# Performance work log

Hardware: AMD Instinct MI355X
Metric: run time of the kernel (lower is better)

Reference implementation:

```python
import jax, jax.numpy as jnp
import numpy as np
from functools import partial

# ---------------- model dims ----------------
B = 1
CIN = 26
COUT = 26
ED = 128              # embed_dim
MLP_HID = 256         # embed_dim * mlp_ratio (2.0)
NLAT, NLON = 361, 720 # model grid
SF = 4                # scale_factor
H, W = NLAT // SF, NLON // SF   # internal SHT grid (90, 180)
LMAX = H              # 90 spherical-harmonic degrees
MMAX = W // 2 + 1     # 91 azimuthal orders
NB = 4                # num_layers
EPS = 1e-6

# ---------------- spherical harmonic transform setup ----------------
def _legendre(lmax, mmax, theta):
    """Orthonormal associated Legendre P_l^m(cos theta), shape [lmax, mmax, nlat].
    Normalized so that int P^2 sin(theta) dtheta = 1/(2*pi)."""
    ct, st = np.cos(theta), np.sin(theta)
    p = np.zeros((lmax, mmax, theta.shape[0]))
    p[0, 0] = np.sqrt(1.0 / (4.0 * np.pi))
    for m in range(1, min(lmax, mmax)):
        p[m, m] = np.sqrt((2 * m + 1) / (2.0 * m)) * st * p[m - 1, m - 1]
    for m in range(mmax):
        if m + 1 < lmax:
            p[m + 1, m] = np.sqrt(2 * m + 3.0) * ct * p[m, m]
        for l in range(m + 2, lmax):
            a = np.sqrt((4.0 * l * l - 1.0) / (l * l - m * m))
            b = np.sqrt(((l - 1.0) ** 2 - m * m) / (4.0 * (l - 1.0) ** 2 - 1.0))
            p[l, m] = a * (ct * p[l - 1, m] - b * p[l - 2, m])
    return p

def _grid(nlat):
    theta = np.pi * (np.arange(nlat) + 0.5) / nlat   # equiangular midpoints
    w = (np.pi / nlat) * np.sin(theta)               # quadrature weights
    return theta, w

_thf, _wf = _grid(NLAT)
_ths, _ws = _grid(H)
_pf = _legendre(LMAX, MMAX, _thf)
_ps = _legendre(LMAX, MMAX, _ths)
PCT_FULL = jnp.asarray(_pf, jnp.float32)
PCTW_FULL = jnp.asarray(_pf * _wf, jnp.float32)
PCT_SMALL = jnp.asarray(_ps, jnp.float32)
PCTW_SMALL = jnp.asarray(_ps * _ws, jnp.float32)

def _sht(x, pctw, nlon):
    # x: [B,C,nlat,nlon] real -> coeffs [B,C,LMAX,MMAX] complex
    F = jnp.fft.rfft(x, axis=-1)[..., :MMAX] * (2.0 * np.pi / nlon)
    return jnp.einsum('lmt,bctm->bclm', pctw, F)

def _isht(c, pct, nlon):
    # c: [B,C,LMAX,MMAX] complex -> [B,C,nlat_out,nlon] real
    g = jnp.einsum('lmt,bclm->bctm', pct, c)
    return jnp.fft.irfft(g, n=nlon, axis=-1, norm='forward')

# ---------------- elementwise / channel-mixing helpers ----------------
_gelu = partial(jax.nn.gelu, approximate=False)

def _inorm(x, g, b):
    # InstanceNorm2d, affine, eps=1e-6, biased variance over spatial dims
    mu = jnp.mean(x, axis=(-2, -1), keepdims=True)
    var = jnp.var(x, axis=(-2, -1), keepdims=True)
    return (x - mu) * jax.lax.rsqrt(var + EPS) * g[:, None, None] + b[:, None, None]

def _conv1x1(x, w, b=None):
    y = jnp.einsum('oc,bchw->bohw', w, x)
    return y if b is None else y + b[:, None, None]

# ---------------- SFNO forward ----------------
def _forward(x, w_enc0, b_enc0, w_enc1, w_spec_r, w_spec_i, g0, b0, g1, b1,
             w_mlp1, b_mlp1, w_mlp2, b_mlp2, w_skip, w_dec0, b_dec0, w_dec1):
    big_res = x
    # encoder: conv1x1 -> gelu -> conv1x1 (no bias)
    x = _conv1x1(_gelu(_conv1x1(x, w_enc0, b_enc0)), w_enc1)
    # per-block transform configs: first block full->small, last small->full
    fwd_t = [(PCTW_FULL, NLON), (PCTW_SMALL, W), (PCTW_SMALL, W), (PCTW_SMALL, W)]
    inv_t = [(PCT_SMALL, W), (PCT_SMALL, W), (PCT_SMALL, W), (PCT_FULL, NLON)]
    scale_res = [True, False, False, True]
    for i in range(NB):
        pw, nli = fwd_t[i]
        pi, nlo = inv_t[i]
        c = _sht(x, pw, nli)                              # [B,ED,LMAX,MMAX]
        # diagonal-in-l spectral conv (dhconv): complex weight shared over m
        wspec = w_spec_r[i] + 1j * w_spec_i[i]            # [ED,ED,LMAX]
        xf = _isht(jnp.einsum('bilm,oil->bolm', c, wspec), pi, nlo)
        # residual: resample through SHT when grids differ, else identity
        res = _isht(c, pi, nlo) if scale_res[i] else x
        h = _inorm(xf, g0[i], b0[i])                      # norm0 (no inner skip)
        h = _gelu(h)                                      # act_layer0
        h = _conv1x1(_gelu(_conv1x1(h, w_mlp1[i], b_mlp1[i])), w_mlp2[i], b_mlp2[i])
        h = _inorm(h, g1[i], b1[i])                       # norm1
        x = h + _conv1x1(res, w_skip[i])                  # outer_skip='linear'
    # big skip: concat input channels, then decoder
    x = jnp.concatenate([x, big_res], axis=1)
    x = _conv1x1(_gelu(_conv1x1(x, w_dec0, b_dec0)), w_dec1)
    return x

# ---------------- harness ----------------
def setup_inputs() -> dict:
    key = jax.random.key(0)
    ks = jax.random.split(key, 12)
    rn = lambda k, shp, std: jax.random.normal(k, shp, jnp.float32) * std
    return {
        'x': rn(ks[0], (B, CIN, NLAT, NLON), 1.0),
        'w_enc0': rn(ks[1], (ED, CIN), (1.0 / CIN) ** 0.5),
        'b_enc0': jnp.zeros((ED,), jnp.float32),
        'w_enc1': rn(ks[2], (ED, ED), (1.0 / ED) ** 0.5),
        'w_spec_r': rn(ks[3], (NB, ED, ED, LMAX), (1.0 / ED) ** 0.5),
        'w_spec_i': rn(ks[4], (NB, ED, ED, LMAX), (1.0 / ED) ** 0.5),
        'g0': jnp.ones((NB, ED), jnp.float32),
        'b0': jnp.zeros((NB, ED), jnp.float32),
        'g1': jnp.ones((NB, ED), jnp.float32),
        'b1': jnp.zeros((NB, ED), jnp.float32),
        'w_mlp1': rn(ks[5], (NB, MLP_HID, ED), (1.0 / ED) ** 0.5),
        'b_mlp1': jnp.zeros((NB, MLP_HID), jnp.float32),
        'w_mlp2': rn(ks[6], (NB, ED, MLP_HID), (1.0 / MLP_HID) ** 0.5),
        'b_mlp2': jnp.zeros((NB, ED), jnp.float32),
        'w_skip': rn(ks[7], (NB, ED, ED), (0.5 / ED) ** 0.5),
        'w_dec0': rn(ks[8], (ED, ED + CIN), (1.0 / (ED + CIN)) ** 0.5),
        'b_dec0': jnp.zeros((ED,), jnp.float32),
        'w_dec1': rn(ks[9], (COUT, ED), (1.0 / ED) ** 0.5),
    }

def reference(x, w_enc0, b_enc0, w_enc1, w_spec_r, w_spec_i, g0, b0, g1, b1,
              w_mlp1, b_mlp1, w_mlp2, b_mlp2, w_skip, w_dec0, b_dec0, w_dec1):
    return _forward(x, w_enc0, b_enc0, w_enc1, w_spec_r, w_spec_i, g0, b0, g1, b1,
                    w_mlp1, b_mlp1, w_mlp2, b_mlp2, w_skip, w_dec0, b_dec0, w_dec1)
```

## Files before the change

### kernel.cpp

```cpp
#include <hip/hip_runtime.h>
#include <math.h>

#ifndef M_PI
#define M_PI 3.14159265358979323846
#endif

#define NLATF 361
#define NLONF 720
#define HSM 90
#define WSM 180
#define LMX 90
#define MM 91
#define EDIM 128
#define CINN 26
#define MLPH 256
#define PFULL (NLATF*NLONF)
#define PSMALL (HSM*WSM)

__device__ __forceinline__ float geluf(float x){
  return 0.5f*x*(1.0f + erff(x*0.70710678118654752440f));
}

__global__ void legendre_kernel(float* __restrict__ pct, int T){
  int idx = blockIdx.x*blockDim.x + threadIdx.x;
  if (idx >= MM*T) return;
  int m = idx / T, t = idx % T;
  double theta = M_PI*((double)t + 0.5)/T;
  double ct = cos(theta), st = sin(theta);
  double pmm = sqrt(1.0/(4.0*M_PI));
  for (int k=1;k<=m;++k) pmm *= sqrt((2.0*k+1.0)/(2.0*k))*st;
  double prev2 = 0.0, prev = 0.0;
  for (int l=0;l<LMX;++l){
    double v;
    if (l < m) v = 0.0;
    else if (l == m) v = pmm;
    else if (l == m+1) v = sqrt(2.0*m+3.0)*ct*pmm;
    else {
      double ll = l, mm2 = (double)m*m;
      double a = sqrt((4.0*ll*ll-1.0)/(ll*ll-mm2));
      double lm1 = (double)(l-1);
      double b = sqrt((lm1*lm1-mm2)/(4.0*lm1*lm1-1.0));
      v = a*(ct*prev - b*prev2);
    }
    pct[((size_t)l*T + t)*MM + m] = (float)v;
    prev2 = prev; prev = v;
  }
}

__global__ void dft_tables_kernel(float* __restrict__ fcos, float* __restrict__ fsin,
                                  float* __restrict__ icos, float* __restrict__ isin, int N){
  int idx = blockIdx.x*blockDim.x + threadIdx.x;
  if (idx >= N*MM) return;
  int n = idx / MM, m = idx % MM;
  int r = (int)(((long long)n*m) % N);
  double ang = 2.0*M_PI*r/N;
  double c = cos(ang), s = sin(ang);
  fcos[(size_t)n*MM+m] = (float)c;
  fsin[(size_t)n*MM+m] = (float)s;
  double w = (m==0) ? 1.0 : ((2*m==N) ? 1.0 : 2.0);
  icos[(size_t)m*N+n] = (float)(w*c);
  isin[(size_t)m*N+n] = (float)(w*s);
}

__global__ __launch_bounds__(128) void dft_fwd_kernel(
    const float* __restrict__ x, float2* __restrict__ Fw,
    const float* __restrict__ fcos, const float* __restrict__ fsin,
    int T, int N){
  __shared__ float xs[4][NLONF];
  int r0 = blockIdx.x*4;
  const float* xp = x + (size_t)r0*N;
  for (int e=threadIdx.x; e<4*N; e+=128) xs[e/N][e%N] = xp[e];
  __syncthreads();
  int m = threadIdx.x;
  if (m >= MM) return;
  float ar[4] = {0,0,0,0}, ai[4] = {0,0,0,0};
  for (int n=0;n<N;++n){
    float c = fcos[(size_t)n*MM+m], s = fsin[(size_t)n*MM+m];
    #pragma unroll
    for (int r=0;r<4;++r){
      float xv = xs[r][n];
      ar[r] = fmaf(xv, c, ar[r]);
      ai[r] = fmaf(-xv, s, ai[r]);
    }
  }
  #pragma unroll
  for (int r=0;r<4;++r){
    int t = (r0+r) % T;
    float sc = (float)((2.0*M_PI/N)*(M_PI/T)*sin(M_PI*((double)t+0.5)/T));
    Fw[(size_t)(r0+r)*MM+m] = make_float2(ar[r]*sc, ai[r]*sc);
  }
}

__global__ __launch_bounds__(128) void dft_fwd_chunk_kernel(
    const float* __restrict__ x, float2* __restrict__ Fw,
    const float* __restrict__ fcos, const float* __restrict__ fsin,
    int Tc, int t0, int Tfull, int N){
  __shared__ float xs[4][NLONF];
  int r0 = blockIdx.x*4;
  const float* xp = x + (size_t)r0*N;
  for (int e=threadIdx.x; e<4*N; e+=128) xs[e/N][e%N] = xp[e];
  __syncthreads();
  int m = threadIdx.x;
  if (m >= MM) return;
  float ar[4] = {0,0,0,0}, ai[4] = {0,0,0,0};
  for (int n=0;n<N;++n){
    float c = fcos[(size_t)n*MM+m], s = fsin[(size_t)n*MM+m];
    #pragma unroll
    for (int r=0;r<4;++r){
      float xv = xs[r][n];
      ar[r] = fmaf(xv, c, ar[r]);
      ai[r] = fmaf(-xv, s, ai[r]);
    }
  }
  #pragma unroll
  for (int r=0;r<4;++r){
    int rr = r0+r;
    int t = t0 + (rr % Tc);
    float sc = (float)((2.0*M_PI/N)*(M_PI/Tfull)*sin(M_PI*((double)t+0.5)/Tfull));
    Fw[(size_t)rr*MM+m] = make_float2(ar[r]*sc, ai[r]*sc);
  }
}

__global__ __launch_bounds__(192) void leg_fwd_kernel(
    const float2* __restrict__ Fw, float2* __restrict__ cc,
    const float* __restrict__ pct, int T){
  int half = threadIdx.x/96, m = threadIdx.x%96;
  int c0 = blockIdx.x*4;
  int l0 = blockIdx.y*6 + half*3;
  if (m >= MM) return;
  float2 acc[3][4];
  #pragma unroll
  for (int j=0;j<3;++j) for (int c=0;c<4;++c) acc[j][c] = make_float2(0.f,0.f);
  for (int t=0;t<T;++t){
    float p[3];
    #pragma unroll
    for (int j=0;j<3;++j) p[j] = pct[((size_t)(l0+j)*T + t)*MM + m];
    #pragma unroll
    for (int c=0;c<4;++c){
      float2 f = Fw[((size_t)(c0+c)*T + t)*MM + m];
      #pragma unroll
      for (int j=0;j<3;++j){
        acc[j][c].x = fmaf(p[j], f.x, acc[j][c].x);
        acc[j][c].y = fmaf(p[j], f.y, acc[j][c].y);
      }
    }
  }
  #pragma unroll
  for (int j=0;j<3;++j)
    #pragma unroll
    for (int c=0;c<4;++c)
      cc[((size_t)(c0+c)*LMX + (l0+j))*MM + m] = acc[j][c];
}

__global__ __launch_bounds__(192) void leg_fwd_acc_kernel(
    const float2* __restrict__ Fw, float2* __restrict__ cc,
    const float* __restrict__ pct, int Tfull, int t0, int Tc){
  int half = threadIdx.x/96, m = threadIdx.x%96;
  int c0 = blockIdx.x*4;
  int l0 = blockIdx.y*6 + half*3;
  if (m >= MM) return;
  float2 acc[3][4];
  #pragma unroll
  for (int j=0;j<3;++j) for (int c=0;c<4;++c) acc[j][c] = make_float2(0.f,0.f);
  for (int tl=0; tl<Tc; ++tl){
    float p[3];
    #pragma unroll
    for (int j=0;j<3;++j) p[j] = pct[((size_t)(l0+j)*Tfull + t0+tl)*MM + m];
    #pragma unroll
    for (int c=0;c<4;++c){
      float2 f = Fw[((size_t)(c0+c)*Tc + tl)*MM + m];
      #pragma unroll
      for (int j=0;j<3;++j){
        acc[j][c].x = fmaf(p[j], f.x, acc[j][c].x);
        acc[j][c].y = fmaf(p[j], f.y, acc[j][c].y);
      }
    }
  }
  #pragma unroll
  for (int j=0;j<3;++j)
    #pragma unroll
    for (int c=0;c<4;++c){
      size_t idx = ((size_t)(c0+c)*LMX + (l0+j))*MM + m;
      cc[idx].x += acc[j][c].x;
      cc[idx].y += acc[j][c].y;
    }
}

__global__ __launch_bounds__(192) void leg_inv_kernel(
    const float2* __restrict__ cc, float2* __restrict__ g,
    const float* __restrict__ pct, int T){
  int half = threadIdx.x/96, m = threadIdx.x%96;
  int c0 = blockIdx.x*4;
  int t0 = blockIdx.y*6 + half*3;
  if (m >= MM) return;
  float2 acc[3][4];
  #pragma unroll
  for (int j=0;j<3;++j) for (int c=0;c<4;++c) acc[j][c] = make_float2(0.f,0.f);
  for (int l=0;l<LMX;++l){
    float p[3];
    #pragma unroll
    for (int j=0;j<3;++j){
      int t = t0+j;
      p[j] = (t<T) ? pct[((size_t)l*T + t)*MM + m] : 0.f;
    }
    #pragma unroll
    for (int c=0;c<4;++c){
      float2 f = cc[((size_t)(c0+c)*LMX + l)*MM + m];
      #pragma unroll
      for (int j=0;j<3;++j){
        acc[j][c].x = fmaf(p[j], f.x, acc[j][c].x);
        acc[j][c].y = fmaf(p[j], f.y, acc[j][c].y);
      }
    }
  }
  #pragma unroll
  for (int j=0;j<3;++j){
    int t = t0+j;
    if (t < T)
      #pragma unroll
      for (int c=0;c<4;++c)
        g[((size_t)(c0+c)*T + t)*MM + m] = acc[j][c];
  }
}

__global__ __launch_bounds__(192) void leg_inv_chunk_kernel(
    const float2* __restrict__ cc, float2* __restrict__ g,
    const float* __restrict__ pct, int Tfull, int t0, int Tc){
  int half = threadIdx.x/96, m = threadIdx.x%96;
  int c0 = blockIdx.x*4;
  int tl0 = blockIdx.y*6 + half*3;
  if (m >= MM) return;
  float2 acc[3][4];
  #pragma unroll
  for (int j=0;j<3;++j) for (int c=0;c<4;++c) acc[j][c] = make_float2(0.f,0.f);
  for (int l=0;l<LMX;++l){
    float p[3];
    #pragma unroll
    for (int j=0;j<3;++j){
      int tl = tl0+j;
      p[j] = (tl<Tc) ? pct[((size_t)l*Tfull + t0+tl)*MM + m] : 0.f;
    }
    #pragma unroll
    for (int c=0;c<4;++c){
      float2 f = cc[((size_t)(c0+c)*LMX + l)*MM + m];
      #pragma unroll
      for (int j=0;j<3;++j){
        acc[j][c].x = fmaf(p[j], f.x, acc[j][c].x);
        acc[j][c].y = fmaf(p[j], f.y, acc[j][c].y);
      }
    }
  }
  #pragma unroll
  for (int j=0;j<3;++j){
    int tl = tl0+j;
    if (tl < Tc)
      #pragma unroll
      for (int c=0;c<4;++c)
        g[((size_t)(c0+c)*Tc + tl)*MM + m] = acc[j][c];
  }
}

__global__ __launch_bounds__(192) void spec_conv_kernel(
    const float2* __restrict__ cc, float2* __restrict__ cc2,
    const float* __restrict__ wr, const float* __restrict__ wi){
  int half = threadIdx.x/96, m = threadIdx.x%96;
  int o0 = blockIdx.x*8;
  int l = blockIdx.y*2 + half;
  if (m >= MM) return;
  float2 acc[8];
  #pragma unroll
  for (int o=0;o<8;++o) acc[o] = make_float2(0.f,0.f);
  for (int i=0;i<EDIM;++i){
    float2 xv = cc[((size_t)i*LMX + l)*MM + m];
    #pragma unroll
    for (int o=0;o<8;++o){
      float wrv = wr[((size_t)(o0+o)*EDIM + i)*LMX + l];
      float wiv = wi[((size_t)(o0+o)*EDIM + i)*LMX + l];
      acc[o].x += wrv*xv.x - wiv*xv.y;
      acc[o].y += wrv*xv.y + wiv*xv.x;
    }
  }
  #pragma unroll
  for (int o=0;o<8;++o) cc2[((size_t)(o0+o)*LMX + l)*MM + m] = acc[o];
}

template<int COLS>
__global__ __launch_bounds__(192) void idft_kernel(
    const float2* __restrict__ g, float* __restrict__ xout,
    const float* __restrict__ icos, const float* __restrict__ isin, int N){
  __shared__ float2 gs[8][MM];
  int r0 = blockIdx.x*8;
  for (int e=threadIdx.x; e<8*MM; e+=192) gs[e/MM][e%MM] = g[(size_t)r0*MM + e];
  __syncthreads();
  float acc[8][COLS];
  #pragma unroll
  for (int r=0;r<8;++r) for (int c=0;c<COLS;++c) acc[r][c] = 0.f;
  for (int m=0;m<MM;++m){
    float tc[COLS], ts[COLS];
    #pragma unroll
    for (int c=0;c<COLS;++c){
      int n = threadIdx.x + c*192;
      tc[c] = (n<N) ? icos[(size_t)m*N+n] : 0.f;
      ts[c] = (n<N) ? isin[(size_t)m*N+n] : 0.f;
    }
    #pragma unroll
    for (int r=0;r<8;++r){
      float2 gv = gs[r][m];
      #pragma unroll
      for (int c=0;c<COLS;++c)
        acc[r][c] = fmaf(gv.x, tc[c], fmaf(-gv.y, ts[c], acc[r][c]));
    }
  }
  #pragma unroll
  for (int r=0;r<8;++r)
    #pragma unroll
    for (int c=0;c<COLS;++c){
      int n = threadIdx.x + c*192;
      if (n<N) xout[(size_t)(r0+r)*N + n] = acc[r][c];
    }
}

__global__ __launch_bounds__(192) void idft_chunk_kernel(
    const float2* __restrict__ g, float* __restrict__ xout,
    const float* __restrict__ icos, const float* __restrict__ isin,
    int Tc, int t0, int Tfull, int N){
  __shared__ float2 gs[8][MM];
  int r0 = blockIdx.x*8;
  for (int e=threadIdx.x; e<8*MM; e+=192){
    int rr = r0 + e/MM;
    int c_ = rr/Tc, tl = rr%Tc;
    gs[e/MM][e%MM] = g[((size_t)c_*Tfull + t0 + tl)*MM + (e%MM)];
  }
  __syncthreads();
  float acc[8][4];
  #pragma unroll
  for (int r=0;r<8;++r) for (int c=0;c<4;++c) acc[r][c] = 0.f;
  for (int m=0;m<MM;++m){
    float tc[4], ts[4];
    #pragma unroll
    for (int c=0;c<4;++c){
      int n = threadIdx.x + c*192;
      tc[c] = (n<N) ? icos[(size_t)m*N+n] : 0.f;
      ts[c] = (n<N) ? isin[(size_t)m*N+n] : 0.f;
    }
    #pragma unroll
    for (int r=0;r<8;++r){
      float2 gv = gs[r][m];
      #pragma unroll
      for (int c=0;c<4;++c)
        acc[r][c] = fmaf(gv.x, tc[c], fmaf(-gv.y, ts[c], acc[r][c]));
    }
  }
  #pragma unroll
  for (int r=0;r<8;++r)
    #pragma unroll
    for (int c=0;c<4;++c){
      int n = threadIdx.x + c*192;
      if (n<N) xout[(size_t)(r0+r)*N + n] = acc[r][c];
    }
}

__global__ __launch_bounds__(256) void stats_kernel(
    const float* __restrict__ x, float* __restrict__ mean, float* __restrict__ rstd, int P){
  int c = blockIdx.x;
  const float* xp = x + (size_t)c*P;
  float s = 0.f, s2 = 0.f;
  for (int p=threadIdx.x; p<P; p+=256){ float v = xp[p]; s += v; s2 = fmaf(v,v,s2); }
  __shared__ float rs[256], rq[256];
  rs[threadIdx.x] = s; rq[threadIdx.x] = s2;
  __syncthreads();
  for (int st=128; st>0; st>>=1){
    if (threadIdx.x < st){ rs[threadIdx.x] += rs[threadIdx.x+st]; rq[threadIdx.x] += rq[threadIdx.x+st]; }
    __syncthreads();
  }
  if (threadIdx.x == 0){
    float mu = rs[0]/P;
    float var = rq[0]/P - mu*mu;
    mean[c] = mu;
    rstd[c] = rsqrtf(fmaxf(var, 0.f) + 1e-6f);
  }
}

__global__ __launch_bounds__(256) void stats_partial_kernel(
    const float* __restrict__ x, long long ld, int P,
    float* __restrict__ s1, float* __restrict__ s2){
  int c = blockIdx.x;
  const float* xp = x + (size_t)c*ld;
  float a = 0.f, b = 0.f;
  for (int p=threadIdx.x; p<P; p+=256){ float v = xp[p]; a += v; b = fmaf(v,v,b); }
  __shared__ float rs[256], rq[256];
  rs[threadIdx.x] = a; rq[threadIdx.x] = b;
  __syncthreads();
  for (int st=128; st>0; st>>=1){
    if (threadIdx.x < st){ rs[threadIdx.x] += rs[threadIdx.x+st]; rq[threadIdx.x] += rq[threadIdx.x+st]; }
    __syncthreads();
  }
  if (threadIdx.x == 0){ s1[c] += rs[0]; s2[c] += rq[0]; }
}

__global__ __launch_bounds__(256) void pstats_kernel(
    const float2* __restrict__ g, int Tc, float Nn,
    float* __restrict__ s1, float* __restrict__ s2){
  int c = blockIdx.x;
  const float2* gp = g + (size_t)c*Tc*MM;
  float a = 0.f, b = 0.f;
  for (int i=threadIdx.x; i<Tc*MM; i+=256){
    int m = i % MM;
    float2 v = gp[i];
    if (m == 0){ a += v.x; b = fmaf(Nn*v.x, v.x, b); }
    else b += 2.f*Nn*(v.x*v.x + v.y*v.y);
  }
  __shared__ float rs[256], rq[256];
  rs[threadIdx.x] = a; rq[threadIdx.x] = b;
  __syncthreads();
  for (int st=128; st>0; st>>=1){
    if (threadIdx.x < st){ rs[threadIdx.x] += rs[threadIdx.x+st]; rq[threadIdx.x] += rq[threadIdx.x+st]; }
    __syncthreads();
  }
  if (threadIdx.x == 0){ s1[c] += rs[0]*Nn; s2[c] += rq[0]; }
}

__global__ void finalize_stats_kernel(
    const float* __restrict__ s1, const float* __restrict__ s2,
    float* __restrict__ mean, float* __restrict__ rstd, float c1){
  int c = threadIdx.x;
  float mu = s1[c]*c1;
  float var = s2[c]*c1 - mu*mu;
  mean[c] = mu;
  rstd[c] = rsqrtf(fmaxf(var, 0.f) + 1e-6f);
}

__global__ void diag_kernel(float* out, float v){ out[0] = v; }

template<bool INNG, bool BIAS, bool GOUT, bool ADDN>
__global__ __launch_bounds__(256) void conv1x1_kernel(
    const float* __restrict__ W, const float* __restrict__ X,
    const float* __restrict__ X2, int K1,
    float* __restrict__ Y, const float* __restrict__ bias,
    const float* __restrict__ nm, const float* __restrict__ nr,
    const float* __restrict__ ng, const float* __restrict__ nb,
    const float* __restrict__ H2,
    int O, int K, int P,
    long long ldx, long long ldx2, long long ldy, long long ldh){
  __shared__ __align__(16) float Wt[16][64];
  __shared__ __align__(16) float Xt[16][64];
  int tid = threadIdx.x;
  int p0 = blockIdx.x*64, o0 = blockIdx.y*64;
  float acc[4][4] = {{0.f}};
  for (int k0=0; k0<K; k0+=16){
    #pragma unroll
    for (int j=0;j<4;++j){
      int e = tid + j*256;
      int ko = e>>6, idx = e&63;
      int o = o0+idx, k = k0+ko;
      Wt[ko][idx] = (o<O && k<K) ? W[(size_t)o*K + k] : 0.f;
    }
    #pragma unroll
    for (int j=0;j<4;++j){
      int e = tid + j*256;
      int ko = e>>6, idx = e&63;
      int k = k0+ko, p = p0+idx;
      float v = 0.f;
      if (k<K && p<P){
        v = (k<K1) ? X[(long long)k*ldx + p] : X2[(long long)(k-K1)*ldx2 + p];
        if (INNG){ v = (v - nm[k])*nr[k]*ng[k] + nb[k]; v = geluf(v); }
      }
      Xt[ko][idx] = v;
    }
    __syncthreads();
    int ty = tid>>4, tx = tid&15;
    #pragma unroll
    for (int kk=0; kk<16; ++kk){
      const float4 av = *(const float4*)(&Wt[kk][ty*4]);
      const float4 bv = *(const float4*)(&Xt[kk][tx*4]);
      acc[0][0] = fmaf(av.x,bv.x,acc[0][0]); acc[0][1] = fmaf(av.x,bv.y,acc[0][1]);
      acc[0][2] = fmaf(av.x,bv.z,acc[0][2]); acc[0][3] = fmaf(av.x,bv.w,acc[0][3]);
      acc[1][0] = fmaf(av.y,bv.x,acc[1][0]); acc[1][1] = fmaf(av.y,bv.y,acc[1][1]);
      acc[1][2] = fmaf(av.y,bv.z,acc[1][2]); acc[1][3] = fmaf(av.y,bv.w,acc[1][3]);
      acc[2][0] = fmaf(av.z,bv.x,acc[2][0]); acc[2][1] = fmaf(av.z,bv.y,acc[2][1]);
      acc[2][2] = fmaf(av.z,bv.z,acc[2][2]); acc[2][3] = fmaf(av.z,bv.w,acc[2][3]);
      acc[3][0] = fmaf(av.w,bv.x,acc[3][0]); acc[3][1] = fmaf(av.w,bv.y,acc[3][1]);
      acc[3][2] = fmaf(av.w,bv.z,acc[3][2]); acc[3][3] = fmaf(av.w,bv.w,acc[3][3]);
    }
    __syncthreads();
  }
  int ty = tid>>4, tx = tid&15;
  #pragma unroll
  for (int i2=0;i2<4;++i2){
    int o = o0+ty*4+i2;
    if (o >= O) continue;
    float bi = BIAS ? bias[o] : 0.f;
    float mu=0.f, rr=0.f, gg=0.f, bb=0.f;
    if (ADDN){ mu = nm[o]; rr = nr[o]; gg = ng[o]; bb = nb[o]; }
    #pragma unroll
    for (int j2=0;j2<4;++j2){
      int p = p0+tx*4+j2;
      if (p >= P) continue;
      float v = acc[i2][j2] + bi;
      if (GOUT) v = geluf(v);
      if (ADDN) v += (H2[(long long)o*ldh + p]-mu)*rr*gg + bb;
      Y[(long long)o*ldy + p] = v;
    }
  }
}

extern "C" void kernel_launch(void* const* d_in, const int* in_sizes, int n_in,
                              void* d_out, int out_size, void* d_ws, size_t ws_size,
                              hipStream_t stream){
  const float* x_in    = (const float*)d_in[0];
  const float* w_enc0  = (const float*)d_in[1];
  const float* b_enc0  = (const float*)d_in[2];
  const float* w_enc1  = (const float*)d_in[3];
  const float* w_spec_r= (const float*)d_in[4];
  const float* w_spec_i= (const float*)d_in[5];
  const float* g0      = (const float*)d_in[6];
  const float* b0      = (const float*)d_in[7];
  const float* g1      = (const float*)d_in[8];
  const float* b1      = (const float*)d_in[9];
  const float* w_mlp1  = (const float*)d_in[10];
  const float* b_mlp1  = (const float*)d_in[11];
  const float* w_mlp2  = (const float*)d_in[12];
  const float* b_mlp2  = (const float*)d_in[13];
  const float* w_skip  = (const float*)d_in[14];
  const float* w_dec0  = (const float*)d_in[15];
  const float* b_dec0  = (const float*)d_in[16];
  const float* w_dec1  = (const float*)d_in[17];
  float* out = (float*)d_out;

  float* ws = (float*)d_ws;
  size_t off = 0;
  auto alloc = [&](size_t n)->float*{ float* p = ws + off; off += (n + 63) & ~(size_t)63; return p; };
  auto asz = [](size_t n)->size_t{ return (n + 63) & ~(size_t)63; };

  float* pctF = alloc((size_t)LMX*NLATF*MM);
  float* pctS = alloc((size_t)LMX*HSM*MM);
  float* fcF = alloc((size_t)NLONF*MM);  float* fsF = alloc((size_t)NLONF*MM);
  float* icF = alloc((size_t)MM*NLONF);  float* isF = alloc((size_t)MM*NLONF);
  float* fcS = alloc((size_t)WSM*MM);    float* fsS = alloc((size_t)WSM*MM);
  float* icS = alloc((size_t)MM*WSM);    float* isS = alloc((size_t)MM*WSM);
  float* CCb  = alloc((size_t)EDIM*LMX*MM*2);
  float* CC2b = alloc((size_t)EDIM*LMX*MM*2);
  float* SMB  = alloc((size_t)EDIM*HSM*MM*2);
  float* XS0  = alloc((size_t)EDIM*PSMALL);
  float* XS1  = alloc((size_t)EDIM*PSMALL);
  float* XFS  = alloc((size_t)EDIM*PSMALL);
  float* RESS = alloc((size_t)EDIM*PSMALL);
  float* sacc = alloc(256);
  float* sm0 = alloc(128); float* sr0 = alloc(128);
  float* sm1 = alloc(128); float* sr1 = alloc(128);
  float* smean = alloc(128); float* srstd = alloc(128);
  size_t base_f = off;
  size_t budget_f = ws_size / sizeof(float);

  struct Cfg { int nc; bool high; bool gf; };
  const Cfg cands[] = {
    {4,false,true},{5,false,true},{6,false,true},{8,false,true},
    {12,false,true},{19,false,true},{19,false,false}
  };
  int nc = -1; bool high=false, gf=false;
  size_t slabT=0, Pslab=0;
  for (const Cfg& c : cands){
    size_t sT = (NLATF + c.nc - 1) / c.nc;
    size_t Ps = sT * NLONF;
    size_t hid_f = asz((size_t)MLPH * (Ps > (size_t)PSMALL ? Ps : (size_t)PSMALL));
    size_t need = base_f + hid_f
                + asz((size_t)EDIM*Ps)
                + asz((size_t)EDIM*Ps)
                + asz((size_t)EDIM*sT*MM*2)
                + (c.gf   ? asz((size_t)EDIM*NLATF*MM*2) : 0)
                + (c.high ? asz((size_t)EDIM*PFULL) : asz((size_t)EDIM*Ps));
    if (need <= budget_f){ nc=c.nc; high=c.high; gf=c.gf; slabT=sT; Pslab=Ps; break; }
  }
  if (nc < 0){
    diag_kernel<<<1,1,0,stream>>>(out, (float)(ws_size >> 20));
    return;
  }
  float* HID  = alloc((size_t)MLPH * (Pslab > (size_t)PSMALL ? Pslab : (size_t)PSMALL));
  float* XFC  = alloc((size_t)EDIM*Pslab);
  float* RESC = alloc((size_t)EDIM*Pslab);
  float* GCb  = alloc((size_t)EDIM*slabT*MM*2);
  float* GFb  = gf ? alloc((size_t)EDIM*NLATF*MM*2) : GCb;
  float* H2S  = high ? alloc((size_t)EDIM*PFULL) : alloc((size_t)EDIM*Pslab);

  float2* CC  = (float2*)CCb;
  float2* CC2 = (float2*)CC2b;
  float2* SM  = (float2*)SMB;
  float2* GC  = (float2*)GCb;
  float2* GF  = (float2*)GFb;

  legendre_kernel<<<(MM*NLATF+255)/256, 256, 0, stream>>>(pctF, NLATF);
  legendre_kernel<<<(MM*HSM+255)/256, 256, 0, stream>>>(pctS, HSM);
  dft_tables_kernel<<<(NLONF*MM+255)/256, 256, 0, stream>>>(fcF, fsF, icF, isF, NLONF);
  dft_tables_kernel<<<(WSM*MM+255)/256, 256, 0, stream>>>(fcS, fsS, icS, isS, WSM);

  enum { CV_PLAIN, CV_BG, CV_INNG_BG, CV_B, CV_ADDN };
  auto conv = [&](int mode, const float* W, const float* X, const float* X2, int K1,
                  float* Y, const float* bias, const float* nm, const float* nr,
                  const float* ng, const float* nb, const float* H2,
                  int O, int K, int P,
                  long long ldx, long long ldx2, long long ldy, long long ldh){
    dim3 g((P+63)/64, (O+63)/64), b(256);
    switch(mode){
      case CV_PLAIN:   conv1x1_kernel<false,false,false,false><<<g,b,0,stream>>>(W,X,X2,K1,Y,bias,nm,nr,ng,nb,H2,O,K,P,ldx,ldx2,ldy,ldh); break;
      case CV_BG:      conv1x1_kernel<false,true, true, false><<<g,b,0,stream>>>(W,X,X2,K1,Y,bias,nm,nr,ng,nb,H2,O,K,P,ldx,ldx2,ldy,ldh); break;
      case CV_INNG_BG: conv1x1_kernel<true, true, true, false><<<g,b,0,stream>>>(W,X,X2,K1,Y,bias,nm,nr,ng,nb,H2,O,K,P,ldx,ldx2,ldy,ldh); break;
      case CV_B:       conv1x1_kernel<false,true, false,false><<<g,b,0,stream>>>(W,X,X2,K1,Y,bias,nm,nr,ng,nb,H2,O,K,P,ldx,ldx2,ldy,ldh); break;
      case CV_ADDN:    conv1x1_kernel<false,false,false,true ><<<g,b,0,stream>>>(W,X,X2,K1,Y,bias,nm,nr,ng,nb,H2,O,K,P,ldx,ldx2,ldy,ldh); break;
    }
  };

  hipMemsetAsync(CCb, 0, (size_t)EDIM*LMX*MM*2*sizeof(float), stream);
  for (int i=0; i<nc; ++i){
    int t0 = i*(int)slabT;
    int Tc = (t0 + (int)slabT <= NLATF) ? (int)slabT : (NLATF - t0);
    int P = Tc*NLONF;
    const float* xin_c = x_in + (size_t)t0*NLONF;
    conv(CV_BG,    w_enc0, xin_c, xin_c, CINN, HID, b_enc0, 0,0,0,0, 0,
         EDIM, CINN, P, PFULL, PFULL, P, P);
    conv(CV_PLAIN, w_enc1, HID, HID, EDIM, XFC, 0, 0,0,0,0, 0,
         EDIM, EDIM, P, P, P, P, P);
    dft_fwd_chunk_kernel<<<(EDIM*Tc)/4, 128, 0, stream>>>(XFC, GC, fcF, fsF, Tc, t0, NLATF, NLONF);
    leg_fwd_acc_kernel<<<dim3(32,15), 192, 0, stream>>>(GC, CC, pctF, NLATF, t0, Tc);
  }

  auto mlp_skip_small = [&](int blk, const float* res, float* xout){
    stats_kernel<<<EDIM,256,0,stream>>>(XFS, smean, srstd, PSMALL);
    conv(CV_INNG_BG, w_mlp1 + (size_t)blk*MLPH*EDIM, XFS, XFS, EDIM, HID,
         b_mlp1 + blk*MLPH, smean, srstd, g0 + blk*EDIM, b0 + blk*EDIM, 0,
         MLPH, EDIM, PSMALL, PSMALL, PSMALL, PSMALL, PSMALL);
    conv(CV_B, w_mlp2 + (size_t)blk*EDIM*MLPH, HID, HID, MLPH, XFS,
         b_mlp2 + blk*EDIM, 0,0,0,0, 0,
         EDIM, MLPH, PSMALL, PSMALL, PSMALL, PSMALL, PSMALL);
    stats_kernel<<<EDIM,256,0,stream>>>(XFS, smean, srstd, PSMALL);
    conv(CV_ADDN, w_skip + (size_t)blk*EDIM*EDIM, res, res, EDIM, xout,
         0, smean, srstd, g1 + blk*EDIM, b1 + blk*EDIM, XFS,
         EDIM, EDIM, PSMALL, PSMALL, PSMALL, PSMALL, PSMALL);
  };

  const size_t SPOFF = (size_t)EDIM*EDIM*LMX;

  spec_conv_kernel<<<dim3(16,45), 192, 0, stream>>>(CC, CC2, w_spec_r, w_spec_i);
  leg_inv_kernel<<<dim3(32,15), 192, 0, stream>>>(CC2, SM, pctS, HSM);
  idft_kernel<1><<<(EDIM*HSM)/8, 192, 0, stream>>>(SM, XFS, icS, isS, WSM);
  leg_inv_kernel<<<dim3(32,15), 192, 0, stream>>>(CC, SM, pctS, HSM);
  idft_kernel<1><<<(EDIM*HSM)/8, 192, 0, stream>>>(SM, RESS, icS, isS, WSM);
  mlp_skip_small(0, RESS, XS0);

  for (int blk=1; blk<=2; ++blk){
    float* xin  = (blk==1) ? XS0 : XS1;
    float* xout = (blk==1) ? XS1 : XS0;
    dft_fwd_kernel<<<(EDIM*HSM)/4, 128, 0, stream>>>(xin, SM, fcS, fsS, HSM, WSM);
    leg_fwd_kernel<<<dim3(32,15), 192, 0, stream>>>(SM, CC, pctS, HSM);
    spec_conv_kernel<<<dim3(16,45), 192, 0, stream>>>(CC, CC2, w_spec_r + blk*SPOFF, w_spec_i + blk*SPOFF);
    leg_inv_kernel<<<dim3(32,15), 192, 0, stream>>>(CC2, SM, pctS, HSM);
    idft_kernel<1><<<(EDIM*HSM)/8, 192, 0, stream>>>(SM, XFS, icS, isS, WSM);
    mlp_skip_small(blk, xin, xout);
  }

  dft_fwd_kernel<<<(EDIM*HSM)/4, 128, 0, stream>>>(XS0, SM, fcS, fsS, HSM, WSM);
  leg_fwd_kernel<<<dim3(32,15), 192, 0, stream>>>(SM, CC, pctS, HSM);
  spec_conv_kernel<<<dim3(16,45), 192, 0, stream>>>(CC, CC2, w_spec_r + 3*SPOFF, w_spec_i + 3*SPOFF);

  hipMemsetAsync(sacc, 0, 256*sizeof(float), stream);
  if (gf){
    leg_inv_kernel<<<dim3(32,61), 192, 0, stream>>>(CC2, GF, pctF, NLATF);
    pstats_kernel<<<EDIM, 256, 0, stream>>>(GF, NLATF, (float)NLONF, sacc, sacc+128);
  } else {
    for (int i=0; i<nc; ++i){
      int t0 = i*(int)slabT;
      int Tc = (t0 + (int)slabT <= NLATF) ? (int)slabT : (NLATF - t0);
      leg_inv_chunk_kernel<<<dim3(32,(Tc+5)/6), 192, 0, stream>>>(CC2, GC, pctF, NLATF, t0, Tc);
      pstats_kernel<<<EDIM, 256, 0, stream>>>(GC, Tc, (float)NLONF, sacc, sacc+128);
    }
  }
  finalize_stats_kernel<<<1,128,0,stream>>>(sacc, sacc+128, sm0, sr0, 1.0f/(float)PFULL);

  hipMemsetAsync(sacc, 0, 256*sizeof(float), stream);
  for (int i=0; i<nc; ++i){
    int t0 = i*(int)slabT;
    int Tc = (t0 + (int)slabT <= NLATF) ? (int)slabT : (NLATF - t0);
    int P = Tc*NLONF;
    if (gf){
      idft_chunk_kernel<<<(EDIM*Tc)/8, 192, 0, stream>>>(GF, XFC, icF, isF, Tc, t0, NLATF, NLONF);
    } else {
      leg_inv_chunk_kernel<<<dim3(32,(Tc+5)/6), 192, 0, stream>>>(CC2, GC, pctF, NLATF, t0, Tc);
      idft_kernel<4><<<(EDIM*Tc)/8, 192, 0, stream>>>(GC, XFC, icF, isF, NLONF);
    }
    conv(CV_INNG_BG, w_mlp1 + 3*(size_t)MLPH*EDIM, XFC, XFC, EDIM, HID,
         b_mlp1 + 3*MLPH, sm0, sr0, g0 + 3*EDIM, b0 + 3*EDIM, 0,
         MLPH, EDIM, P, P, P, P, P);
    float* h2dst = high ? (H2S + (size_t)t0*NLONF) : H2S;
    long long ldh2 = high ? (long long)PFULL : (long long)P;
    conv(CV_B, w_mlp2 + 3*(size_t)EDIM*MLPH, HID, HID, MLPH, h2dst,
         b_mlp2 + 3*EDIM, 0,0,0,0, 0,
         EDIM, MLPH, P, P, P, ldh2, P);
    stats_partial_kernel<<<EDIM, 256, 0, stream>>>(h2dst, ldh2, P, sacc, sacc+128);
  }
  finalize_stats_kernel<<<1,128,0,stream>>>(sacc, sacc+128, sm1, sr1, 1.0f/(float)PFULL);

  if (gf) leg_inv_kernel<<<dim3(32,61), 192, 0, stream>>>(CC, GF, pctF, NLATF);
  for (int i=0; i<nc; ++i){
    int t0 = i*(int)slabT;
    int Tc = (t0 + (int)slabT <= NLATF) ? (int)slabT : (NLATF - t0);
    int P = Tc*NLONF;
    if (gf){
      idft_chunk_kernel<<<(EDIM*Tc)/8, 192, 0, stream>>>(GF, RESC, icF, isF, Tc, t0, NLATF, NLONF);
    } else {
      leg_inv_chunk_kernel<<<dim3(32,(Tc+5)/6), 192, 0, stream>>>(CC, GC, pctF, NLATF, t0, Tc);
      idft_kernel<4><<<(EDIM*Tc)/8, 192, 0, stream>>>(GC, RESC, icF, isF, NLONF);
    }
    const float* h2src; long long ldh2;
    if (high){
      h2src = H2S + (size_t)t0*NLONF; ldh2 = PFULL;
    } else {
      leg_inv_chunk_kernel<<<dim3(32,(Tc+5)/6), 192, 0, stream>>>(CC2, GC, pctF, NLATF, t0, Tc);
      idft_kernel<4><<<(EDIM*Tc)/8, 192, 0, stream>>>(GC, XFC, icF, isF, NLONF);
      conv(CV_INNG_BG, w_mlp1 + 3*(size_t)MLPH*EDIM, XFC, XFC, EDIM, HID,
           b_mlp1 + 3*MLPH, sm0, sr0, g0 + 3*EDIM, b0 + 3*EDIM, 0,
           MLPH, EDIM, P, P, P, P, P);
      conv(CV_B, w_mlp2 + 3*(size_t)EDIM*MLPH, HID, HID, MLPH, H2S,
           b_mlp2 + 3*EDIM, 0,0,0,0, 0,
           EDIM, MLPH, P, P, P, P, P);
      h2src = H2S; ldh2 = P;
    }
    conv(CV_ADDN, w_skip + 3*(size_t)EDIM*EDIM, RESC, RESC, EDIM, XFC,
         0, sm1, sr1, g1 + 3*EDIM, b1 + 3*EDIM, h2src,
         EDIM, EDIM, P, P, P, P, ldh2);
    conv(CV_BG, w_dec0, XFC, x_in + (size_t)t0*NLONF, EDIM, HID,
         b_dec0, 0,0,0,0, 0,
         EDIM, EDIM+CINN, P, P, PFULL, P, P);
    conv(CV_PLAIN, w_dec1, HID, HID, EDIM, out + (size_t)t0*NLONF,
         0, 0,0,0,0, 0,
         CINN, EDIM, P, P, P, PFULL, P);
  }
}
```

Baseline: 7.389 ms.

## Enlarge conv and DFT tiles, split norm-GELU into own pass, prefer high config

The 1x1 conv GEMM moves from 64x64 tiles with a 4x4 micro-tile to 128x128 tiles with an 8x8 micro-tile per thread. This raises arithmetic intensity, and strides switch to 32-bit int indexing. The norm+GELU on the input is pulled out of the GEMM load into a separate in-place elementwise kernel, so it runs once per element instead of once per output tile. The forward DFT kernels process 8 rows per block instead of 4, and the workspace config list now tries 'high' (stored full-resolution H2) options first. The costs are higher register pressure and lower occupancy in the conv, fewer blocks on small grids, and an extra memory pass for normalization.

```diff
diff --git a/kernel.cpp b/kernel.cpp
--- a/kernel.cpp
+++ b/kernel.cpp
@@ -66,25 +66,25 @@
     const float* __restrict__ x, float2* __restrict__ Fw,
     const float* __restrict__ fcos, const float* __restrict__ fsin,
     int T, int N){
-  __shared__ float xs[4][NLONF];
-  int r0 = blockIdx.x*4;
+  __shared__ float xs[8][NLONF];
+  int r0 = blockIdx.x*8;
   const float* xp = x + (size_t)r0*N;
-  for (int e=threadIdx.x; e<4*N; e+=128) xs[e/N][e%N] = xp[e];
+  for (int e=threadIdx.x; e<8*N; e+=128) xs[e/N][e%N] = xp[e];
   __syncthreads();
   int m = threadIdx.x;
   if (m >= MM) return;
-  float ar[4] = {0,0,0,0}, ai[4] = {0,0,0,0};
+  float ar[8] = {0,0,0,0,0,0,0,0}, ai[8] = {0,0,0,0,0,0,0,0};
   for (int n=0;n<N;++n){
     float c = fcos[(size_t)n*MM+m], s = fsin[(size_t)n*MM+m];
     #pragma unroll
-    for (int r=0;r<4;++r){
+    for (int r=0;r<8;++r){
       float xv = xs[r][n];
       ar[r] = fmaf(xv, c, ar[r]);
       ai[r] = fmaf(-xv, s, ai[r]);
     }
   }
   #pragma unroll
-  for (int r=0;r<4;++r){
+  for (int r=0;r<8;++r){
     int t = (r0+r) % T;
     float sc = (float)((2.0*M_PI/N)*(M_PI/T)*sin(M_PI*((double)t+0.5)/T));
     Fw[(size_t)(r0+r)*MM+m] = make_float2(ar[r]*sc, ai[r]*sc);
@@ -95,25 +95,25 @@
     const float* __restrict__ x, float2* __restrict__ Fw,
     const float* __restrict__ fcos, const float* __restrict__ fsin,
     int Tc, int t0, int Tfull, int N){
-  __shared__ float xs[4][NLONF];
-  int r0 = blockIdx.x*4;
+  __shared__ float xs[8][NLONF];
+  int r0 = blockIdx.x*8;
   const float* xp = x + (size_t)r0*N;
-  for (int e=threadIdx.x; e<4*N; e+=128) xs[e/N][e%N] = xp[e];
+  for (int e=threadIdx.x; e<8*N; e+=128) xs[e/N][e%N] = xp[e];
   __syncthreads();
   int m = threadIdx.x;
   if (m >= MM) return;
-  float ar[4] = {0,0,0,0}, ai[4] = {0,0,0,0};
+  float ar[8] = {0,0,0,0,0,0,0,0}, ai[8] = {0,0,0,0,0,0,0,0};
   for (int n=0;n<N;++n){
     float c = fcos[(size_t)n*MM+m], s = fsin[(size_t)n*MM+m];
     #pragma unroll
-    for (int r=0;r<4;++r){
+    for (int r=0;r<8;++r){
       float xv = xs[r][n];
       ar[r] = fmaf(xv, c, ar[r]);
       ai[r] = fmaf(-xv, s, ai[r]);
     }
   }
   #pragma unroll
-  for (int r=0;r<4;++r){
+  for (int r=0;r<8;++r){
     int rr = r0+r;
     int t = t0 + (rr % Tc);
     float sc = (float)((2.0*M_PI/N)*(M_PI/Tfull)*sin(M_PI*((double)t+0.5)/Tfull));
@@ -432,7 +432,23 @@
 
 __global__ void diag_kernel(float* out, float v){ out[0] = v; }
 
-template<bool INNG, bool BIAS, bool GOUT, bool ADDN>
+__global__ __launch_bounds__(256) void ngact_kernel(
+    float* __restrict__ x, const float* __restrict__ mean, const float* __restrict__ rstd,
+    const float* __restrict__ g, const float* __restrict__ b, int P){
+  int c = blockIdx.y;
+  int p = (blockIdx.x*256 + threadIdx.x)*4;
+  if (p >= P) return;
+  float m = mean[c], r = rstd[c]*g[c], bb = b[c];
+  float4* xp = (float4*)(x + (size_t)c*P + p);
+  float4 v = *xp;
+  v.x = geluf((v.x-m)*r + bb);
+  v.y = geluf((v.y-m)*r + bb);
+  v.z = geluf((v.z-m)*r + bb);
+  v.w = geluf((v.w-m)*r + bb);
+  *xp = v;
+}
+
+template<bool BIAS, bool GOUT, bool ADDN>
 __global__ __launch_bounds__(256) void conv1x1_kernel(
     const float* __restrict__ W, const float* __restrict__ X,
     const float* __restrict__ X2, int K1,
@@ -441,65 +457,67 @@
     const float* __restrict__ ng, const float* __restrict__ nb,
     const float* __restrict__ H2,
     int O, int K, int P,
-    long long ldx, long long ldx2, long long ldy, long long ldh){
-  __shared__ __align__(16) float Wt[16][64];
-  __shared__ __align__(16) float Xt[16][64];
+    int ldx, int ldx2, int ldy, int ldh){
+  __shared__ __align__(16) float Wt[16][128];
+  __shared__ __align__(16) float Xt[16][128];
   int tid = threadIdx.x;
-  int p0 = blockIdx.x*64, o0 = blockIdx.y*64;
-  float acc[4][4] = {{0.f}};
+  int p0 = blockIdx.x*128, o0 = blockIdx.y*128;
+  int ty = tid>>4, tx = tid&15;
+  float acc[8][8];
+  #pragma unroll
+  for (int i=0;i<8;++i)
+    #pragma unroll
+    for (int j=0;j<8;++j) acc[i][j] = 0.f;
   for (int k0=0; k0<K; k0+=16){
     #pragma unroll
-    for (int j=0;j<4;++j){
+    for (int j=0;j<8;++j){
       int e = tid + j*256;
-      int ko = e>>6, idx = e&63;
+      int ko = e>>7, idx = e&127;
       int o = o0+idx, k = k0+ko;
-      Wt[ko][idx] = (o<O && k<K) ? W[(size_t)o*K + k] : 0.f;
-    }
-    #pragma unroll
-    for (int j=0;j<4;++j){
+      Wt[ko][idx] = (o<O && k<K) ? W[o*K + k] : 0.f;
+    }
+    #pragma unroll
+    for (int j=0;j<8;++j){
       int e = tid + j*256;
-      int ko = e>>6, idx = e&63;
+      int ko = e>>7, idx = e&127;
       int k = k0+ko, p = p0+idx;
       float v = 0.f;
-      if (k<K && p<P){
-        v = (k<K1) ? X[(long long)k*ldx + p] : X2[(long long)(k-K1)*ldx2 + p];
-        if (INNG){ v = (v - nm[k])*nr[k]*ng[k] + nb[k]; v = geluf(v); }
-      }
+      if (k<K && p<P)
+        v = (k<K1) ? X[k*ldx + p] : X2[(k-K1)*ldx2 + p];
       Xt[ko][idx] = v;
     }
     __syncthreads();
-    int ty = tid>>4, tx = tid&15;
     #pragma unroll
     for (int kk=0; kk<16; ++kk){
-      const float4 av = *(const float4*)(&Wt[kk][ty*4]);
-      const float4 bv = *(const float4*)(&Xt[kk][tx*4]);
-      acc[0][0] = fmaf(av.x,bv.x,acc[0][0]); acc[0][1] = fmaf(av.x,bv.y,acc[0][1]);
-      acc[0][2] = fmaf(av.x,bv.z,acc[0][2]); acc[0][3] = fmaf(av.x,bv.w,acc[0][3]);
-      acc[1][0] = fmaf(av.y,bv.x,acc[1][0]); acc[1][1] = fmaf(av.y,bv.y,acc[1][1]);
-      acc[1][2] = fmaf(av.y,bv.z,acc[1][2]); acc[1][3] = fmaf(av.y,bv.w,acc[1][3]);
-      acc[2][0] = fmaf(av.z,bv.x,acc[2][0]); acc[2][1] = fmaf(av.z,bv.y,acc[2][1]);
-      acc[2][2] = fmaf(av.z,bv.z,acc[2][2]); acc[2][3] = fmaf(av.z,bv.w,acc[2][3]);
-      acc[3][0] = fmaf(av.w,bv.x,acc[3][0]); acc[3][1] = fmaf(av.w,bv.y,acc[3][1]);
-      acc[3][2] = fmaf(av.w,bv.z,acc[3][2]); acc[3][3] = fmaf(av.w,bv.w,acc[3][3]);
+      float4 a0 = *(const float4*)(&Wt[kk][ty*4]);
+      float4 a1 = *(const float4*)(&Wt[kk][64+ty*4]);
+      float4 b0 = *(const float4*)(&Xt[kk][tx*4]);
+      float4 b1 = *(const float4*)(&Xt[kk][64+tx*4]);
+      float a[8] = {a0.x,a0.y,a0.z,a0.w,a1.x,a1.y,a1.z,a1.w};
+      float b[8] = {b0.x,b0.y,b0.z,b0.w,b1.x,b1.y,b1.z,b1.w};
+      #pragma unroll
+      for (int i=0;i<8;++i)
+        #pragma unroll
+        for (int jj=0;jj<8;++jj)
+          acc[i][jj] = fmaf(a[i], b[jj], acc[i][jj]);
     }
     __syncthreads();
   }
-  int ty = tid>>4, tx = tid&15;
-  #pragma unroll
-  for (int i2=0;i2<4;++i2){
-    int o = o0+ty*4+i2;
+  #pragma unroll
+  for (int i=0;i<8;++i){
+    int o = o0 + ((i<4) ? (ty*4+i) : (64+ty*4+i-4));
     if (o >= O) continue;
     float bi = BIAS ? bias[o] : 0.f;
     float mu=0.f, rr=0.f, gg=0.f, bb=0.f;
     if (ADDN){ mu = nm[o]; rr = nr[o]; gg = ng[o]; bb = nb[o]; }
     #pragma unroll
-    for (int j2=0;j2<4;++j2){
-      int p = p0+tx*4+j2;
+    for (int jj=0;jj<8;++jj){
+      int p = p0 + ((jj<4) ? (tx*4+jj) : (64+tx*4+jj-4));
       if (p >= P) continue;
-      float v = acc[i2][j2] + bi;
+      float v = acc[i][jj] + bi;
       if (GOUT) v = geluf(v);
-      if (ADDN) v += (H2[(long long)o*ldh + p]-mu)*rr*gg + bb;
-      Y[(long long)o*ldy + p] = v;
+      if (ADDN) v += (H2[o*ldh + p]-mu)*rr*gg + bb;
+      Y[o*ldy + p] = v;
     }
   }
 }
@@ -554,8 +572,8 @@
 
   struct Cfg { int nc; bool high; bool gf; };
   const Cfg cands[] = {
-    {4,false,true},{5,false,true},{6,false,true},{8,false,true},
-    {12,false,true},{19,false,true},{19,false,false}
+    {8,true,true},{12,true,true},{19,true,true},{19,true,false},
+    {8,false,true},{12,false,true},{19,false,true},{19,false,false}
   };
   int nc = -1; bool high=false, gf=false;
   size_t slabT=0, Pslab=0;
@@ -593,20 +611,22 @@
   dft_tables_kernel<<<(NLONF*MM+255)/256, 256, 0, stream>>>(fcF, fsF, icF, isF, NLONF);
   dft_tables_kernel<<<(WSM*MM+255)/256, 256, 0, stream>>>(fcS, fsS, icS, isS, WSM);
 
-  enum { CV_PLAIN, CV_BG, CV_INNG_BG, CV_B, CV_ADDN };
+  enum { CV_PLAIN, CV_BG, CV_B, CV_ADDN };
   auto conv = [&](int mode, const float* W, const float* X, const float* X2, int K1,
                   float* Y, const float* bias, const float* nm, const float* nr,
                   const float* ng, const float* nb, const float* H2,
-                  int O, int K, int P,
-                  long long ldx, long long ldx2, long long ldy, long long ldh){
-    dim3 g((P+63)/64, (O+63)/64), b(256);
+                  int O, int K, int P, int ldx, int ldx2, int ldy, int ldh){
+    dim3 g((P+127)/128, (O+127)/128), b(256);
     switch(mode){
-      case CV_PLAIN:   conv1x1_kernel<false,false,false,false><<<g,b,0,stream>>>(W,X,X2,K1,Y,bias,nm,nr,ng,nb,H2,O,K,P,ldx,ldx2,ldy,ldh); break;
-      case CV_BG:      conv1x1_kernel<false,true, true, false><<<g,b,0,stream>>>(W,X,X2,K1,Y,bias,nm,nr,ng,nb,H2,O,K,P,ldx,ldx2,ldy,ldh); break;
-      case CV_INNG_BG: conv1x1_kernel<true, true, true, false><<<g,b,0,stream>>>(W,X,X2,K1,Y,bias,nm,nr,ng,nb,H2,O,K,P,ldx,ldx2,ldy,ldh); break;
-      case CV_B:       conv1x1_kernel<false,true, false,false><<<g,b,0,stream>>>(W,X,X2,K1,Y,bias,nm,nr,ng,nb,H2,O,K,P,ldx,ldx2,ldy,ldh); break;
-      case CV_ADDN:    conv1x1_kernel<false,false,false,true ><<<g,b,0,stream>>>(W,X,X2,K1,Y,bias,nm,nr,ng,nb,H2,O,K,P,ldx,ldx2,ldy,ldh); break;
-    }
+      case CV_PLAIN: conv1x1_kernel<false,false,false><<<g,b,0,stream>>>(W,X,X2,K1,Y,bias,nm,nr,ng,nb,H2,O,K,P,ldx,ldx2,ldy,ldh); break;
+      case CV_BG:    conv1x1_kernel<true, true, false><<<g,b,0,stream>>>(W,X,X2,K1,Y,bias,nm,nr,ng,nb,H2,O,K,P,ldx,ldx2,ldy,ldh); break;
+      case CV_B:     conv1x1_kernel<true, false,false><<<g,b,0,stream>>>(W,X,X2,K1,Y,bias,nm,nr,ng,nb,H2,O,K,P,ldx,ldx2,ldy,ldh); break;
+      case CV_ADDN:  conv1x1_kernel<false,false,true ><<<g,b,0,stream>>>(W,X,X2,K1,Y,bias,nm,nr,ng,nb,H2,O,K,P,ldx,ldx2,ldy,ldh); break;
+    }
+  };
+  auto ngact = [&](float* x, const float* mean, const float* rstd,
+                   const float* g, const float* b, int P){
+    ngact_kernel<<<dim3((P/4+255)/256, EDIM), 256, 0, stream>>>(x, mean, rstd, g, b, P);
   };
 
   hipMemsetAsync(CCb, 0, (size_t)EDIM*LMX*MM*2*sizeof(float), stream);
@@ -619,14 +639,15 @@
          EDIM, CINN, P, PFULL, PFULL, P, P);
     conv(CV_PLAIN, w_enc1, HID, HID, EDIM, XFC, 0, 0,0,0,0, 0,
          EDIM, EDIM, P, P, P, P, P);
-    dft_fwd_chunk_kernel<<<(EDIM*Tc)/4, 128, 0, stream>>>(XFC, GC, fcF, fsF, Tc, t0, NLATF, NLONF);
+    dft_fwd_chunk_kernel<<<(EDIM*Tc)/8, 128, 0, stream>>>(XFC, GC, fcF, fsF, Tc, t0, NLATF, NLONF);
     leg_fwd_acc_kernel<<<dim3(32,15), 192, 0, stream>>>(GC, CC, pctF, NLATF, t0, Tc);
   }
 
   auto mlp_skip_small = [&](int blk, const float* res, float* xout){
     stats_kernel<<<EDIM,256,0,stream>>>(XFS, smean, srstd, PSMALL);
-    conv(CV_INNG_BG, w_mlp1 + (size_t)blk*MLPH*EDIM, XFS, XFS, EDIM, HID,
-         b_mlp1 + blk*MLPH, smean, srstd, g0 + blk*EDIM, b0 + blk*EDIM, 0,
+    ngact(XFS, smean, srstd, g0 + blk*EDIM, b0 + blk*EDIM, PSMALL);
+    conv(CV_BG, w_mlp1 + (size_t)blk*MLPH*EDIM, XFS, XFS, EDIM, HID,
+         b_mlp1 + blk*MLPH, 0,0,0,0, 0,
          MLPH, EDIM, PSMALL, PSMALL, PSMALL, PSMALL, PSMALL);
     conv(CV_B, w_mlp2 + (size_t)blk*EDIM*MLPH, HID, HID, MLPH, XFS,
          b_mlp2 + blk*EDIM, 0,0,0,0, 0,
@@ -649,7 +670,7 @@
   for (int blk=1; blk<=2; ++blk){
     float* xin  = (blk==1) ? XS0 : XS1;
     float* xout = (blk==1) ? XS1 : XS0;
-    dft_fwd_kernel<<<(EDIM*HSM)/4, 128, 0, stream>>>(xin, SM, fcS, fsS, HSM, WSM);
+    dft_fwd_kernel<<<(EDIM*HSM)/8, 128, 0, stream>>>(xin, SM, fcS, fsS, HSM, WSM);
     leg_fwd_kernel<<<dim3(32,15), 192, 0, stream>>>(SM, CC, pctS, HSM);
     spec_conv_kernel<<<dim3(16,45), 192, 0, stream>>>(CC, CC2, w_spec_r + blk*SPOFF, w_spec_i + blk*SPOFF);
     leg_inv_kernel<<<dim3(32,15), 192, 0, stream>>>(CC2, SM, pctS, HSM);
@@ -657,7 +678,7 @@
     mlp_skip_small(blk, xin, xout);
   }
 
-  dft_fwd_kernel<<<(EDIM*HSM)/4, 128, 0, stream>>>(XS0, SM, fcS, fsS, HSM, WSM);
+  dft_fwd_kernel<<<(EDIM*HSM)/8, 128, 0, stream>>>(XS0, SM, fcS, fsS, HSM, WSM);
   leg_fwd_kernel<<<dim3(32,15), 192, 0, stream>>>(SM, CC, pctS, HSM);
   spec_conv_kernel<<<dim3(16,45), 192, 0, stream>>>(CC, CC2, w_spec_r + 3*SPOFF, w_spec_i + 3*SPOFF);
 
@@ -686,11 +707,12 @@
       leg_inv_chunk_kernel<<<dim3(32,(Tc+5)/6), 192, 0, stream>>>(CC2, GC, pctF, NLATF, t0, Tc);
       idft_kernel<4><<<(EDIM*Tc)/8, 192, 0, stream>>>(GC, XFC, icF, isF, NLONF);
     }
-    conv(CV_INNG_BG, w_mlp1 + 3*(size_t)MLPH*EDIM, XFC, XFC, EDIM, HID,
-         b_mlp1 + 3*MLPH, sm0, sr0, g0 + 3*EDIM, b0 + 3*EDIM, 0,
+    ngact(XFC, sm0, sr0, g0 + 3*EDIM, b0 + 3*EDIM, P);
+    conv(CV_BG, w_mlp1 + 3*(size_t)MLPH*EDIM, XFC, XFC, EDIM, HID,
+         b_mlp1 + 3*MLPH, 0,0,0,0, 0,
          MLPH, EDIM, P, P, P, P, P);
     float* h2dst = high ? (H2S + (size_t)t0*NLONF) : H2S;
-    long long ldh2 = high ? (long long)PFULL : (long long)P;
+    int ldh2 = high ? PFULL : P;
     conv(CV_B, w_mlp2 + 3*(size_t)EDIM*MLPH, HID, HID, MLPH, h2dst,
          b_mlp2 + 3*EDIM, 0,0,0,0, 0,
          EDIM, MLPH, P, P, P, ldh2, P);
@@ -709,14 +731,15 @@
       leg_inv_chunk_kernel<<<dim3(32,(Tc+5)/6), 192, 0, stream>>>(CC, GC, pctF, NLATF, t0, Tc);
       idft_kernel<4><<<(EDIM*Tc)/8, 192, 0, stream>>>(GC, RESC, icF, isF, NLONF);
     }
-    const float* h2src; long long ldh2;
+    const float* h2src; int ldh2;
     if (high){
       h2src = H2S + (size_t)t0*NLONF; ldh2 = PFULL;
     } else {
       leg_inv_chunk_kernel<<<dim3(32,(Tc+5)/6), 192, 0, stream>>>(CC2, GC, pctF, NLATF, t0, Tc);
       idft_kernel<4><<<(EDIM*Tc)/8, 192, 0, stream>>>(GC, XFC, icF, isF, NLONF);
-      conv(CV_INNG_BG, w_mlp1 + 3*(size_t)MLPH*EDIM, XFC, XFC, EDIM, HID,
-           b_mlp1 + 3*MLPH, sm0, sr0, g0 + 3*EDIM, b0 + 3*EDIM, 0,
+      ngact(XFC, sm0, sr0, g0 + 3*EDIM, b0 + 3*EDIM, P);
+      conv(CV_BG, w_mlp1 + 3*(size_t)MLPH*EDIM, XFC, XFC, EDIM, HID,
+           b_mlp1 + 3*MLPH, 0,0,0,0, 0,
            MLPH, EDIM, P, P, P, P, P);
       conv(CV_B, w_mlp2 + 3*(size_t)EDIM*MLPH, HID, HID, MLPH, H2S,
            b_mlp2 + 3*EDIM, 0,0,0,0, 0,
```

Result: slower. 16.20 ms (+119.2%).
